# Optimization experiments

Measured on AMD Instinct MI355X. Metric: run time of the kernel, lower is better.

Reference implementation:

```python
import jax, jax.numpy as jnp
import numpy as np

MODEL_DIM = 1024
NUM_HEADS = 16
HEAD_DIM = MODEL_DIM // NUM_HEADS
ROPE_BASE = 10000.0


def apply_rope_full(x):
    # RoPE applied over the FULL model_dim (before head split), interleaved pairs.
    B, S, D = x.shape
    half = D // 2
    inv_freq = 1.0 / (ROPE_BASE ** (jnp.arange(half, dtype=x.dtype) / half))  # [half]
    ang = jnp.arange(S, dtype=x.dtype)[:, None] * inv_freq[None, :]           # [S, half]
    cos, sin = jnp.cos(ang), jnp.sin(ang)
    x1 = x[..., 0::2]  # [B,S,half]
    x2 = x[..., 1::2]
    r1 = x1 * cos - x2 * sin
    r2 = x1 * sin + x2 * cos
    # re-interleave
    return jnp.stack([r1, r2], axis=-1).reshape(B, S, D)


def setup_inputs() -> dict:
    key = jax.random.key(0)
    ks = jax.random.split(key, 9)
    B, S, D = 4, 2048, MODEL_DIM
    sc = 1.0 / np.sqrt(D)
    inp = {
        "X": jax.random.normal(ks[0], (B, S, D), dtype=jnp.float32),
        "Wq": jax.random.normal(ks[1], (D, D), dtype=jnp.float32) * sc,
        "bq": jnp.zeros((D,), dtype=jnp.float32),
        "Wk": jax.random.normal(ks[2], (D, D), dtype=jnp.float32) * sc,
        "bk": jnp.zeros((D,), dtype=jnp.float32),
        "Wv": jax.random.normal(ks[3], (D, D), dtype=jnp.float32) * sc,
        "bv": jnp.zeros((D,), dtype=jnp.float32),
        "Wo": jax.random.normal(ks[4], (D, D), dtype=jnp.float32) * sc,
        "bo": jnp.zeros((D,), dtype=jnp.float32),
    }
    return inp


def reference(X, Wq, bq, Wk, bk, Wv, bv, Wo, bo):
    B, S, D = X.shape
    H, hd = NUM_HEADS, HEAD_DIM
    q = apply_rope_full(X @ Wq + bq)  # [B,S,D], RoPE on full dim as in source
    k = apply_rope_full(X @ Wk + bk)
    v = X @ Wv + bv
    # split heads (contiguous slices d1:d2 == reshape to [B,S,H,hd])
    qh = q.reshape(B, S, H, hd)
    kh = k.reshape(B, S, H, hd)
    vh = v.reshape(B, S, H, hd)
    scale = 1.0 / jnp.sqrt(jnp.asarray(hd, dtype=X.dtype))
    scores = jnp.einsum("bqhd,bkhd->bhqk", qh, kh) * scale  # [B,H,S,S]
    causal = jnp.tril(jnp.ones((S, S), dtype=bool))
    scores = jnp.where(causal[None, None], scores, -jnp.inf)
    weights = jax.nn.softmax(scores, axis=-1)
    attn = jnp.einsum("bhqk,bkhd->bqhd", weights, vh).reshape(B, S, D)
    return attn @ Wo + bo
```

## Files before the change

### kernel.cpp

```cpp
#include <hip/hip_runtime.h>

typedef unsigned short u16;
typedef unsigned int   u32;
typedef __attribute__((ext_vector_type(4))) float f32x4;
typedef __attribute__((ext_vector_type(8))) short short8;

#define MODEL_DIM 1024
#define SEQ 2048
#define BATCH 4
#define NHEAD 16
#define HDIM 64
#define MTOT (BATCH*SEQ)
#define ELEMS ((size_t)MTOT*MODEL_DIM)

__device__ __forceinline__ u16 f2bf(float f) {
    u32 u = __float_as_uint(f);
    u = (u + 0x7fffu + ((u >> 16) & 1u)) >> 16;
    return (u16)u;
}
__device__ __forceinline__ u32 pack2(float a, float b) {
    return (u32)f2bf(a) | ((u32)f2bf(b) << 16);
}
__device__ __forceinline__ u32 cvtpk(float lo, float hi) {
    u32 r;
    asm("v_cvt_pk_bf16_f32 %0, %1, %2" : "=v"(r) : "v"(lo), "v"(hi));
    return r;
}
__device__ __forceinline__ float exp2a(float x) {
    float r;
    asm("v_exp_f32 %0, %1" : "=v"(r) : "v"(x));
    return r;
}

#define GLOAD16(g, l) __builtin_amdgcn_global_load_lds(                        \
        (const __attribute__((address_space(1))) unsigned int*)(g),            \
        (__attribute__((address_space(3))) unsigned int*)(l), 16, 0, 0)

__global__ __launch_bounds__(256) void prep_k(const float* __restrict__ X,
                                              u16* __restrict__ Xb,
                                              const float* __restrict__ Wq,
                                              const float* __restrict__ Wk,
                                              const float* __restrict__ Wv,
                                              const float* __restrict__ Wo,
                                              u16* __restrict__ Wt) {
    const int bid = blockIdx.x, t = threadIdx.x;
    if (bid < 8192) {
        size_t i = ((size_t)bid * 256 + t) * 4;
        float4 v = *(const float4*)(X + i);
        uint2 o; o.x = pack2(v.x, v.y); o.y = pack2(v.z, v.w);
        *(uint2*)(Xb + i) = o;
        return;
    }
    __shared__ float tile[32][33];
    const int bid2 = bid - 8192;
    const int z = bid2 >> 10, rem = bid2 & 1023;
    const int by = rem >> 5, bx = rem & 31;
    const float* W = (z == 0) ? Wq : (z == 1) ? Wk : (z == 2) ? Wv : Wo;
    const int k0 = by * 32, n0 = bx * 32;
    const int x = t & 31, y = t >> 5;
    for (int i = 0; i < 4; ++i)
        tile[y + i * 8][x] = W[(size_t)(k0 + y + i * 8) * MODEL_DIM + n0 + x];
    __syncthreads();
    u16* out = Wt + ((size_t)z << 20);
    for (int i = 0; i < 4; ++i)
        out[(size_t)(n0 + y + i * 8) * MODEL_DIM + k0 + x] = f2bf(tile[x][y + i * 8]);
}

template<int MODE>
__global__ __launch_bounds__(256) void gemm128_k(
        const u16* __restrict__ A, const u16* __restrict__ Wt,
        u16* __restrict__ Qb, u16* __restrict__ Kb, u32* __restrict__ VT,
        float* __restrict__ outO,
        const float* __restrict__ bq, const float* __restrict__ bk,
        const float* __restrict__ bv, const float* __restrict__ bo) {
    __shared__ __align__(16) u16 smem[(MODE == 0) ? 128 * 130 : 128 * 64];
    u16* As = smem;
    u16* Bs = smem + 4096;
    const int tid  = threadIdx.x;
    const int wave = tid >> 6, lane = tid & 63;
    const int l15  = lane & 15, quad = lane >> 4;
    const int wm = (wave & 1) * 64, wn = (wave >> 1) * 64;
    const int m0 = blockIdx.x * 128;
    const int n0 = blockIdx.y * 128;

    const u16* bbase;
    if (MODE == 0) {
        int region = n0 >> 10;
        bbase = Wt + ((size_t)region << 20) + (size_t)(n0 & 1023) * MODEL_DIM;
    } else {
        bbase = Wt + ((size_t)3 << 20) + (size_t)n0 * MODEL_DIM;
    }
    const u16* abase = A + (size_t)m0 * MODEL_DIM;

    f32x4 acc[4][4] = {};
    const int r0 = tid >> 2, kc0 = (tid & 3) * 8;
    const u16* ga = abase + (size_t)r0 * MODEL_DIM + kc0;
    const u16* gb = bbase + (size_t)r0 * MODEL_DIM + kc0;
    u16* la0 = &As[tid * 8];
    u16* la1 = &As[2048 + tid * 8];
    u16* lb0 = &Bs[tid * 8];
    u16* lb1 = &Bs[2048 + tid * 8];

    for (int k0 = 0; k0 < MODEL_DIM; k0 += 32) {
        GLOAD16(ga + k0, la0);
        GLOAD16(ga + (size_t)64 * MODEL_DIM + k0, la1);
        GLOAD16(gb + k0, lb0);
        GLOAD16(gb + (size_t)64 * MODEL_DIM + k0, lb1);
        __syncthreads();
        short8 af[4], bf[4];
        for (int i = 0; i < 4; ++i)
            af[i] = *(const short8*)(&As[(wm + i * 16 + l15) * 32 + quad * 8]);
        for (int i = 0; i < 4; ++i)
            bf[i] = *(const short8*)(&Bs[(wn + i * 16 + l15) * 32 + quad * 8]);
        for (int mi = 0; mi < 4; ++mi)
            for (int ni = 0; ni < 4; ++ni)
                acc[mi][ni] = __builtin_amdgcn_mfma_f32_16x16x32_bf16(
                                  af[mi], bf[ni], acc[mi][ni], 0, 0, 0);
        __syncthreads();
    }

    if (MODE == 0) {
        const int region = n0 >> 10;
        if (region < 2) {
            const float* bias = (region == 0) ? bq : bk;
            u16* dst = (region == 0) ? Qb : Kb;
            const float qsc = (region == 0) ? 0.125f * 1.44269504f : 1.0f;
            const float cfr = -0.017989922f;
            float invf[4];
            for (int ni = 0; ni < 4; ++ni) {
                int c = (n0 + wn + ni * 16 + l15) & 1023;
                invf[ni] = __expf((float)(c >> 1) * cfr);
            }
            const float sgn = (l15 & 1) ? 1.0f : -1.0f;
            for (int mi = 0; mi < 4; ++mi)
                for (int r = 0; r < 4; ++r) {
                    size_t rowg = (size_t)(m0 + wm + mi * 16 + quad * 4 + r);
                    float fs = (float)(int)(rowg & 2047);
                    for (int ni = 0; ni < 4; ++ni) {
                        int c = (n0 + wn + ni * 16 + l15) & 1023;
                        float v = acc[mi][ni][r] + bias[c];
                        float mate = __shfl_xor(v, 1, 64);
                        float sn, cs;
                        __sincosf(fs * invf[ni], &sn, &cs);
                        float o = (v * cs + sgn * mate * sn) * qsc;
                        dst[rowg * MODEL_DIM + c] = f2bf(o);
                    }
                }
        } else {
            u16* Ts = smem;
            for (int mi = 0; mi < 4; ++mi)
                for (int r = 0; r < 4; ++r) {
                    int rl = wm + mi * 16 + quad * 4 + r;
                    for (int ni = 0; ni < 4; ++ni) {
                        int cl = wn + ni * 16 + l15;
                        Ts[cl * 130 + rl] = f2bf(acc[mi][ni][r]
                                                 + bv[(n0 & 1023) + cl]);
                    }
                }
            __syncthreads();
            const int b_ = m0 >> 11;
            const int srow0 = (m0 & 2047) >> 1;
            const int h0 = (n0 & 1023) >> 6;
            u32* vtb = VT + (size_t)((b_ * NHEAD + h0) * HDIM) * (SEQ / 2);
            for (int it = 0; it < 32; ++it) {
                int idx = it * 256 + tid;
                int dl = idx >> 6, sc = idx & 63;
                u32 val = *(const u32*)&Ts[dl * 130 + 2 * sc];
                vtb[(size_t)dl * (SEQ / 2) + srow0 + sc] = val;
            }
        }
    } else {
        for (int mi = 0; mi < 4; ++mi)
            for (int r = 0; r < 4; ++r) {
                size_t rowg = (size_t)(m0 + wm + mi * 16 + quad * 4 + r);
                for (int ni = 0; ni < 4; ++ni) {
                    int colg = n0 + wn + ni * 16 + l15;
                    outO[rowg * MODEL_DIM + colg] = acc[mi][ni][r] + bo[colg];
                }
            }
    }
}

__global__ __launch_bounds__(256, 2) void attn_k(const u16* __restrict__ Qb,
                                                 const u16* __restrict__ Kb,
                                                 const u32* __restrict__ VT32,
                                                 u16* __restrict__ Ob) {
    __shared__ __align__(16) u16 Ks[2][64 * 64];
    __shared__ __align__(16) u16 Vs[2][64 * 64];
    __shared__ __align__(16) u16 Pl[4 * 32 * 72];
    const int tid  = threadIdx.x;
    const int wave = tid >> 6, lane = tid & 63;
    const int l15  = lane & 15, quad = lane >> 4;
    const int j = blockIdx.x;
    const int h = blockIdx.y, b = blockIdx.z;
    u16* pw = &Pl[wave * 32 * 72];

    const int key0 = tid >> 3;
    const int c8   = (tid & 7) * 8;
    const int c4   = (tid & 7) * 4;
    const int lko  = key0 * 64 + (((tid & 7) ^ (key0 & 7)) * 8);
    const u16* kgp = Kb + (size_t)(b * SEQ) * MODEL_DIM + h * HDIM;
    const u32* vgp = VT32 + (size_t)((b * NHEAD + h) * HDIM) * (SEQ / 2);

    int bufc = 0;
    for (int pp = 0; pp < 2; ++pp) {
        const int qt = pp ? j : 15 - j;
        const int q0 = qt * 128;
        const int qbase = q0 + wave * 32;

        short8 qfr[2][2];
        for (int qf = 0; qf < 2; ++qf)
            for (int ks = 0; ks < 2; ++ks)
                qfr[qf][ks] = *(const short8*)(Qb
                    + (size_t)(b * SEQ + qbase + qf * 16 + l15) * MODEL_DIM
                    + h * HDIM + ks * 32 + quad * 8);

        float m_i[2] = {-1e30f, -1e30f}, l_i[2] = {0.f, 0.f};
        f32x4 o_acc[4][2] = {};

        const int nkt = (q0 + 128) >> 6;
        uint4 kr0 = *(const uint4*)(kgp + (size_t)key0 * MODEL_DIM + c8);
        uint4 kr1 = *(const uint4*)(kgp + (size_t)(key0 + 32) * MODEL_DIM + c8);
        uint4 vr0 = *(const uint4*)(vgp + (size_t)key0 * (SEQ / 2) + c4);
        uint4 vr1 = *(const uint4*)(vgp + (size_t)(key0 + 32) * (SEQ / 2) + c4);

        for (int kt = 0; kt < nkt; ++kt) {
            const int k0 = kt * 64;
            u16* ksb = Ks[bufc];
            u16* vsb = Vs[bufc];
            *(uint4*)(&ksb[lko])        = kr0;
            *(uint4*)(&ksb[lko + 2048]) = kr1;
            *(uint4*)(&vsb[lko])        = vr0;
            *(uint4*)(&vsb[lko + 2048]) = vr1;
            __syncthreads();

            if (kt + 1 < nkt) {
                const int kn = k0 + 64;
                kr0 = *(const uint4*)(kgp + (size_t)(kn + key0) * MODEL_DIM + c8);
                kr1 = *(const uint4*)(kgp + (size_t)(kn + key0 + 32) * MODEL_DIM + c8);
                vr0 = *(const uint4*)(vgp + (size_t)key0 * (SEQ / 2) + (kn >> 1) + c4);
                vr1 = *(const uint4*)(vgp + (size_t)(key0 + 32) * (SEQ / 2)
                                      + (kn >> 1) + c4);
            }

            if (k0 <= qbase + 31) {
                f32x4 s[4][2] = {};
                for (int ks = 0; ks < 2; ++ks) {
                    short8 kfr[4];
                    for (int kf = 0; kf < 4; ++kf)
                        kfr[kf] = *(const short8*)(&ksb[(kf * 16 + l15) * 64
                                      + (((ks * 4 + quad) ^ (l15 & 7)) * 8)]);
                    for (int kf = 0; kf < 4; ++kf)
                        for (int qf = 0; qf < 2; ++qf)
                            s[kf][qf] = __builtin_amdgcn_mfma_f32_16x16x32_bf16(
                                            kfr[kf], qfr[qf][ks], s[kf][qf], 0, 0, 0);
                }
                for (int qf = 0; qf < 2; ++qf) {
                    int qg = qbase + qf * 16 + l15;
                    if (k0 + 63 > qbase + qf * 16) {
                        for (int kf = 0; kf < 4; ++kf)
                            for (int r = 0; r < 4; ++r)
                                if (k0 + kf * 16 + quad * 4 + r > qg)
                                    s[kf][qf][r] = -1e30f;
                    }
                    float t0 = fmaxf(fmaxf(s[0][qf][0], s[0][qf][1]),
                                     fmaxf(s[0][qf][2], s[0][qf][3]));
                    float t1 = fmaxf(fmaxf(s[1][qf][0], s[1][qf][1]),
                                     fmaxf(s[1][qf][2], s[1][qf][3]));
                    float t2 = fmaxf(fmaxf(s[2][qf][0], s[2][qf][1]),
                                     fmaxf(s[2][qf][2], s[2][qf][3]));
                    float t3 = fmaxf(fmaxf(s[3][qf][0], s[3][qf][1]),
                                     fmaxf(s[3][qf][2], s[3][qf][3]));
                    float rmax = fmaxf(fmaxf(t0, t1), fmaxf(t2, t3));
                    rmax = fmaxf(rmax, __shfl_xor(rmax, 16, 64));
                    rmax = fmaxf(rmax, __shfl_xor(rmax, 32, 64));
                    if (!__all(rmax <= m_i[qf] + 8.0f)) {
                        float mn = fmaxf(m_i[qf], rmax);
                        float alpha = exp2a(m_i[qf] - mn);
                        m_i[qf] = mn;
                        l_i[qf] *= alpha;
                        for (int dt = 0; dt < 4; ++dt)
                            for (int r = 0; r < 4; ++r) o_acc[dt][qf][r] *= alpha;
                    }
                    float mref = m_i[qf];
                    float psum = 0.f;
                    for (int kf = 0; kf < 4; ++kf)
                        for (int r = 0; r < 4; ++r) {
                            float p = exp2a(s[kf][qf][r] - mref);
                            s[kf][qf][r] = p;
                            psum += p;
                        }
                    psum += __shfl_xor(psum, 16, 64);
                    psum += __shfl_xor(psum, 32, 64);
                    l_i[qf] += psum;
                    for (int kf = 0; kf < 4; ++kf) {
                        uint2 w;
                        w.x = cvtpk(s[kf][qf][0], s[kf][qf][1]);
                        w.y = cvtpk(s[kf][qf][2], s[kf][qf][3]);
                        *(uint2*)(&pw[(qf * 16 + l15) * 72 + kf * 16 + quad * 4]) = w;
                    }
                }
                for (int ks = 0; ks < 2; ++ks) {
                    short8 pfr[2], vfr[4];
                    for (int qf = 0; qf < 2; ++qf)
                        pfr[qf] = *(const short8*)(&pw[(qf * 16 + l15) * 72
                                                       + ks * 32 + quad * 8]);
                    for (int dt = 0; dt < 4; ++dt)
                        vfr[dt] = *(const short8*)(&vsb[(dt * 16 + l15) * 64
                                      + (((ks * 4 + quad) ^ (l15 & 7)) * 8)]);
                    for (int dt = 0; dt < 4; ++dt)
                        for (int qf = 0; qf < 2; ++qf)
                            o_acc[dt][qf] = __builtin_amdgcn_mfma_f32_16x16x32_bf16(
                                                vfr[dt], pfr[qf], o_acc[dt][qf], 0, 0, 0);
                }
            }
            bufc ^= 1;
        }

        for (int qf = 0; qf < 2; ++qf) {
            float rl = 1.f / l_i[qf];
            int q = qbase + qf * 16 + l15;
            for (int dt = 0; dt < 4; ++dt) {
                uint2 w;
                w.x = cvtpk(o_acc[dt][qf][0] * rl, o_acc[dt][qf][1] * rl);
                w.y = cvtpk(o_acc[dt][qf][2] * rl, o_acc[dt][qf][3] * rl);
                *(uint2*)(&Ob[(size_t)(b * SEQ + q) * MODEL_DIM
                              + h * HDIM + dt * 16 + quad * 4]) = w;
            }
        }
    }
}

extern "C" void kernel_launch(void* const* d_in, const int* in_sizes, int n_in,
                              void* d_out, int out_size, void* d_ws, size_t ws_size,
                              hipStream_t stream) {
    const float* X  = (const float*)d_in[0];
    const float* Wq = (const float*)d_in[1];
    const float* bq = (const float*)d_in[2];
    const float* Wk = (const float*)d_in[3];
    const float* bk = (const float*)d_in[4];
    const float* Wv = (const float*)d_in[5];
    const float* bv = (const float*)d_in[6];
    const float* Wo = (const float*)d_in[7];
    const float* bo = (const float*)d_in[8];
    float* out = (float*)d_out;

    char* ws = (char*)d_ws;
    u16* Xb   = (u16*)ws;
    u16* Ob   = (u16*)ws;
    u16* Wt   = (u16*)(ws + 16777216);
    u16* Qb   = (u16*)(ws + 25165824);
    u16* Kb   = (u16*)(ws + 41943040);
    u32* VT32 = (u32*)(ws + 75497472);

    prep_k<<<dim3(12288), dim3(256), 0, stream>>>(X, Xb, Wq, Wk, Wv, Wo, Wt);
    gemm128_k<0><<<dim3(64, 24), dim3(256), 0, stream>>>(Xb, Wt, Qb, Kb, VT32,
                                                         nullptr, bq, bk, bv, nullptr);
    attn_k<<<dim3(8, 16, 4), dim3(256), 0, stream>>>(Qb, Kb, VT32, Ob);
    gemm128_k<1><<<dim3(64, 8), dim3(256), 0, stream>>>(Ob, Wt, nullptr, nullptr,
                                                        nullptr, out,
                                                        nullptr, nullptr, nullptr, bo);
}
```

Measured before the change: 271.6 us.

## Move V transpose into separate kernel, shrink GEMM LDS, add MFMA priority hints

The QKV GEMM now writes V row-major to a new buffer instead of transposing through a large LDS tile in its epilogue, and a new vt_k kernel builds the transposed V layout. This cuts the GEMM's shared memory from 128x130 to 2x128x32 elements, which may raise occupancy. The cost is an extra launch and an extra round trip of V through global memory. Separately, s_setprio is placed around the MFMA blocks in the attention kernel to favour waves issuing matrix ops.

After: 277.2 us. +2.1%, slower.

```diff
diff --git a/kernel.cpp b/kernel.cpp
--- a/kernel.cpp
+++ b/kernel.cpp
@@ -69,13 +69,12 @@
 template<int MODE>
 __global__ __launch_bounds__(256) void gemm128_k(
         const u16* __restrict__ A, const u16* __restrict__ Wt,
-        u16* __restrict__ Qb, u16* __restrict__ Kb, u32* __restrict__ VT,
+        u16* __restrict__ Qb, u16* __restrict__ Kb, u16* __restrict__ Vb,
         float* __restrict__ outO,
         const float* __restrict__ bq, const float* __restrict__ bk,
         const float* __restrict__ bv, const float* __restrict__ bo) {
-    __shared__ __align__(16) u16 smem[(MODE == 0) ? 128 * 130 : 128 * 64];
-    u16* As = smem;
-    u16* Bs = smem + 4096;
+    __shared__ __align__(16) u16 As[128 * 32];
+    __shared__ __align__(16) u16 Bs[128 * 32];
     const int tid  = threadIdx.x;
     const int wave = tid >> 6, lane = tid & 63;
     const int l15  = lane & 15, quad = lane >> 4;
@@ -147,27 +146,14 @@
                     }
                 }
         } else {
-            u16* Ts = smem;
             for (int mi = 0; mi < 4; ++mi)
                 for (int r = 0; r < 4; ++r) {
-                    int rl = wm + mi * 16 + quad * 4 + r;
+                    size_t rowg = (size_t)(m0 + wm + mi * 16 + quad * 4 + r);
                     for (int ni = 0; ni < 4; ++ni) {
-                        int cl = wn + ni * 16 + l15;
-                        Ts[cl * 130 + rl] = f2bf(acc[mi][ni][r]
-                                                 + bv[(n0 & 1023) + cl]);
-                    }
-                }
-            __syncthreads();
-            const int b_ = m0 >> 11;
-            const int srow0 = (m0 & 2047) >> 1;
-            const int h0 = (n0 & 1023) >> 6;
-            u32* vtb = VT + (size_t)((b_ * NHEAD + h0) * HDIM) * (SEQ / 2);
-            for (int it = 0; it < 32; ++it) {
-                int idx = it * 256 + tid;
-                int dl = idx >> 6, sc = idx & 63;
-                u32 val = *(const u32*)&Ts[dl * 130 + 2 * sc];
-                vtb[(size_t)dl * (SEQ / 2) + srow0 + sc] = val;
-            }
+                        int col = (n0 + wn + ni * 16 + l15) & 1023;
+                        Vb[rowg * MODEL_DIM + col] = f2bf(acc[mi][ni][r] + bv[col]);
+                    }
+                }
         }
     } else {
         for (int mi = 0; mi < 4; ++mi)
@@ -178,6 +164,30 @@
                     outO[rowg * MODEL_DIM + colg] = acc[mi][ni][r] + bo[colg];
                 }
             }
+    }
+}
+
+__global__ __launch_bounds__(256) void vt_k(const u32* __restrict__ Vb32,
+                                            u32* __restrict__ VT32) {
+    __shared__ u32 tile[64 * 33];
+    int bh = blockIdx.y, b = bh >> 4, h = bh & 15;
+    int s0 = blockIdx.x * 64;
+    int t = threadIdx.x;
+    for (int it = 0; it < 8; ++it) {
+        int idx = it * 256 + t;
+        int s = idx >> 5, dc = idx & 31;
+        tile[s * 33 + dc] = Vb32[(size_t)(b * SEQ + s0 + s) * (MODEL_DIM / 2)
+                                 + h * (HDIM / 2) + dc];
+    }
+    __syncthreads();
+    for (int it = 0; it < 8; ++it) {
+        int idx = it * 256 + t;
+        int d = idx >> 5, sc = idx & 31;
+        u32 w0 = tile[(2 * sc) * 33 + (d >> 1)];
+        u32 w1 = tile[(2 * sc + 1) * 33 + (d >> 1)];
+        u32 val = (d & 1) ? ((w0 >> 16) | (w1 & 0xffff0000u))
+                          : ((w0 & 0xffffu) | (w1 << 16));
+        VT32[(size_t)(bh * HDIM + d) * (SEQ / 2) + (s0 >> 1) + sc] = val;
     }
 }
 
@@ -250,10 +260,12 @@
                     for (int kf = 0; kf < 4; ++kf)
                         kfr[kf] = *(const short8*)(&ksb[(kf * 16 + l15) * 64
                                       + (((ks * 4 + quad) ^ (l15 & 7)) * 8)]);
+                    __builtin_amdgcn_s_setprio(1);
                     for (int kf = 0; kf < 4; ++kf)
                         for (int qf = 0; qf < 2; ++qf)
                             s[kf][qf] = __builtin_amdgcn_mfma_f32_16x16x32_bf16(
                                             kfr[kf], qfr[qf][ks], s[kf][qf], 0, 0, 0);
+                    __builtin_amdgcn_s_setprio(0);
                 }
                 for (int qf = 0; qf < 2; ++qf) {
                     int qg = qbase + qf * 16 + l15;
@@ -308,10 +320,12 @@
                     for (int dt = 0; dt < 4; ++dt)
                         vfr[dt] = *(const short8*)(&vsb[(dt * 16 + l15) * 64
                                       + (((ks * 4 + quad) ^ (l15 & 7)) * 8)]);
+                    __builtin_amdgcn_s_setprio(1);
                     for (int dt = 0; dt < 4; ++dt)
                         for (int qf = 0; qf < 2; ++qf)
                             o_acc[dt][qf] = __builtin_amdgcn_mfma_f32_16x16x32_bf16(
                                                 vfr[dt], pfr[qf], o_acc[dt][qf], 0, 0, 0);
+                    __builtin_amdgcn_s_setprio(0);
                 }
             }
             bufc ^= 1;
@@ -351,11 +365,13 @@
     u16* Wt   = (u16*)(ws + 16777216);
     u16* Qb   = (u16*)(ws + 25165824);
     u16* Kb   = (u16*)(ws + 41943040);
+    u16* Vb   = (u16*)(ws + 58720256);
     u32* VT32 = (u32*)(ws + 75497472);
 
     prep_k<<<dim3(12288), dim3(256), 0, stream>>>(X, Xb, Wq, Wk, Wv, Wo, Wt);
-    gemm128_k<0><<<dim3(64, 24), dim3(256), 0, stream>>>(Xb, Wt, Qb, Kb, VT32,
-                                                         nullptr, bq, bk, bv, nullptr);
+    gemm128_k<0><<<dim3(64, 24), dim3(256), 0, stream>>>(Xb, Wt, Qb, Kb, Vb, nullptr,
+                                                         bq, bk, bv, nullptr);
+    vt_k<<<dim3(32, 64), dim3(256), 0, stream>>>((const u32*)Vb, VT32);
     attn_k<<<dim3(8, 16, 4), dim3(256), 0, stream>>>(Qb, Kb, VT32, Ob);
     gemm128_k<1><<<dim3(64, 8), dim3(256), 0, stream>>>(Ob, Wt, nullptr, nullptr,
                                                         nullptr, out,
```
